# Kernel optimization log

Hardware: AMD Instinct MI355X
Metric: run time of the kernel (lower is better)

The kernel has to match this reference:

```python
import jax, jax.numpy as jnp
import numpy as np

B, S, V, E, H = 256, 512, 800, 128, 256

def setup_inputs() -> dict:
    key = jax.random.key(0)
    ks = jax.random.split(key, 16)
    def rn(k, shape, scale=0.05):
        return jax.random.normal(k, shape, dtype=jnp.float32) * scale
    return {
        "x": jax.random.randint(ks[0], (B, S), 0, V),
        "emb": rn(ks[1], (V, E), 1.0),
        "Wih0": rn(ks[2], (4 * H, E)),
        "Whh0": rn(ks[3], (4 * H, H)),
        "bih0": rn(ks[4], (4 * H,)),
        "bhh0": rn(ks[5], (4 * H,)),
        "Wih1": rn(ks[6], (4 * H, H)),
        "Whh1": rn(ks[7], (4 * H, H)),
        "bih1": rn(ks[8], (4 * H,)),
        "bhh1": rn(ks[9], (4 * H,)),
        "ln_g": jnp.ones((H,), jnp.float32),
        "ln_b": jnp.zeros((H,), jnp.float32),
        "proj_W": rn(ks[10], (E, H)),
        "proj_b": rn(ks[11], (E,)),
    }

def _lstm_layer(x, Wih, Whh, bih, bhh):
    # x: [B, S, D]; returns full hidden sequence [B, S, H]
    b, s, _ = x.shape
    h0 = jnp.zeros((b, H), x.dtype)
    c0 = jnp.zeros((b, H), x.dtype)
    # precompute input projections for all timesteps: [S, B, 4H]
    xp = jnp.einsum("bsd,gd->sbg", x, Wih) + bih + bhh

    def step(carry, xp_t):
        h, c = carry
        gates = xp_t + h @ Whh.T  # [B, 4H]
        i, f, g, o = jnp.split(gates, 4, axis=-1)  # torch gate order i,f,g,o
        i = jax.nn.sigmoid(i)
        f = jax.nn.sigmoid(f)
        g = jnp.tanh(g)
        o = jax.nn.sigmoid(o)
        c = f * c + i * g
        h = o * jnp.tanh(c)
        return (h, c), h

    (_, _), hs = jax.lax.scan(step, (h0, c0), xp)
    return hs.transpose(1, 0, 2)  # [B, S, H]

def reference(x, emb, Wih0, Whh0, bih0, bhh0, Wih1, Whh1, bih1, bhh1, ln_g, ln_b, proj_W, proj_b):
    table = emb.at[0].set(0.0)  # padding_idx=0
    e = table[x]  # [B, S, E]
    h1 = _lstm_layer(e, Wih0, Whh0, bih0, bhh0)
    h2 = _lstm_layer(h1, Wih1, Whh1, bih1, bhh1)
    hn = h2[:, -1, :]  # h_n[-1]: last layer, final timestep [B, H]
    mu = jnp.mean(hn, axis=-1, keepdims=True)
    var = jnp.mean(jnp.square(hn - mu), axis=-1, keepdims=True)
    y = (hn - mu) * jax.lax.rsqrt(var + 1e-5) * ln_g + ln_b
    return y @ proj_W.T + proj_b  # [B, 128]
```

## Files before the change

kernel.cpp:

```cpp
#include <hip/hip_runtime.h>
#include <hip/hip_bf16.h>


typedef unsigned short u16;
typedef unsigned int   u32;
using short8 = __attribute__((ext_vector_type(8))) short;
using f32x4  = __attribute__((ext_vector_type(4))) float;

#define NB 256
#define NS 512
#define NE 128
#define NH 256
#define NG 1024

#define WLDS_FRAGS 18
#define HOFF 147456
#define SCAN_LDS (HOFF + 2 * 16 * NH * 2)

#define L2E     1.4426950408889634f
#define TWO_L2E 2.8853900817779268f

__device__ __forceinline__ u16 f2b(float x) {
  __hip_bfloat16 h = __float2bfloat16(x);
  return __builtin_bit_cast(u16, h);
}
__device__ __forceinline__ float b2f(u16 u) {
  return __builtin_bit_cast(float, (u32)u << 16);
}
__device__ __forceinline__ float ex2(float x)  { return __builtin_amdgcn_exp2f(x); }
__device__ __forceinline__ float ex2n(float x) { return __builtin_amdgcn_exp2f(-x); }
__device__ __forceinline__ float rcpa(float x) { return __builtin_amdgcn_rcpf(x); }

__global__ __launch_bounds__(256) void prep_weights(
    const float* Wih0, const float* Whh0, const float* bih0, const float* bhh0,
    const float* Wih1, const float* Whh1, const float* bih1, const float* bhh1,
    u16* wih0b, u16* whh0b, u16* wih1b, u16* whh1b, float* bc0, float* bc1) {
  int stride = gridDim.x * blockDim.x;
  int tid = blockIdx.x * blockDim.x + threadIdx.x;
  for (int i = tid; i < NG * NE; i += stride) {
    float s = (((i >> 7) >> 8) == 2) ? TWO_L2E : L2E;
    wih0b[i] = f2b(Wih0[i] * s);
  }
  for (int i = tid; i < NG * NH; i += stride) {
    float s = (((i >> 8) >> 8) == 2) ? TWO_L2E : L2E;
    whh0b[i] = f2b(Whh0[i] * s);
    wih1b[i] = f2b(Wih1[i] * s);
    whh1b[i] = f2b(Whh1[i] * s);
  }
  for (int i = tid; i < NG; i += stride) {
    float s = ((i >> 8) == 2) ? TWO_L2E : L2E;
    bc0[i] = (bih0[i] + bhh0[i]) * s;
    bc1[i] = (bih1[i] + bhh1[i]) * s;
  }
}

__global__ __launch_bounds__(256) void embed_chunk(const int* __restrict__ x,
                                                   const float* __restrict__ emb,
                                                   u16* __restrict__ ebuf, int t0) {
  int gid = blockIdx.x * 256 + threadIdx.x;
  int d4 = gid & 31;
  int sb = gid >> 5;
  int b  = sb & (NB - 1);
  int sl = sb >> 8;
  int tok = x[b * NS + (t0 + sl)];
  float4 v = make_float4(0.f, 0.f, 0.f, 0.f);
  if (tok != 0) v = *(const float4*)(emb + (size_t)tok * NE + d4 * 4);
  ushort4 o;
  o.x = f2b(v.x); o.y = f2b(v.y); o.z = f2b(v.z); o.w = f2b(v.w);
  *(ushort4*)(ebuf + (size_t)sb * NE + d4 * 4) = o;
}

template <int K>
__global__ __launch_bounds__(256) void xp_gemm(const u16* __restrict__ A,
                                               const u16* __restrict__ W,
                                               const float* __restrict__ bias,
                                               u16* __restrict__ Cout) {
  __shared__ __align__(16) char lds[2 * 128 * 80];
  char* Asm = lds;
  char* Bsm = lds + 128 * 80;
  int tid = threadIdx.x;
  int w = tid >> 6, l = tid & 63;
  int hi = l >> 4, lo = l & 15;
  int mblk = blockIdx.x >> 3, nblk = blockIdx.x & 7;
  size_t arow0 = (size_t)mblk * 128;
  int g0 = nblk * 128;
  int wm = (w >> 1) * 64, wn = (w & 1) * 64;
  f32x4 acc[4][4] = {};
  int r = tid >> 1, cp = tid & 1;

  for (int k0 = 0; k0 < K; k0 += 32) {
    int4 a0 = *(const int4*)(A + (arow0 + r) * K + k0 + cp * 16);
    int4 a1 = *(const int4*)(A + (arow0 + r) * K + k0 + cp * 16 + 8);
    int4 b0 = *(const int4*)(W + (size_t)(g0 + r) * K + k0 + cp * 16);
    int4 b1 = *(const int4*)(W + (size_t)(g0 + r) * K + k0 + cp * 16 + 8);
    *(int4*)(Asm + r * 80 + cp * 32)      = a0;
    *(int4*)(Asm + r * 80 + cp * 32 + 16) = a1;
    *(int4*)(Bsm + r * 80 + cp * 32)      = b0;
    *(int4*)(Bsm + r * 80 + cp * 32 + 16) = b1;
    __syncthreads();
    short8 af[4], bfr[4];
#pragma unroll
    for (int mt = 0; mt < 4; ++mt)
      af[mt] = *(const short8*)(Asm + (wm + mt * 16 + lo) * 80 + hi * 16);
#pragma unroll
    for (int nt = 0; nt < 4; ++nt)
      bfr[nt] = *(const short8*)(Bsm + (wn + nt * 16 + lo) * 80 + hi * 16);
#pragma unroll
    for (int mt = 0; mt < 4; ++mt)
#pragma unroll
      for (int nt = 0; nt < 4; ++nt)
        acc[mt][nt] = __builtin_amdgcn_mfma_f32_16x16x32_bf16(af[mt], bfr[nt], acc[mt][nt], 0, 0, 0);
    __syncthreads();
  }
#pragma unroll
  for (int nt = 0; nt < 4; ++nt) {
    int gc = g0 + wn + nt * 16 + lo;
    float bv = bias[gc];
    int ws_ = (gc >> 4) & 7, mts = gc >> 7, his = (gc >> 2) & 3, rs = gc & 3;
    size_t gbase = ((size_t)(ws_ * 8 + mts) << 8) + (size_t)(his * 16) * 4 + rs;
#pragma unroll
    for (int mt = 0; mt < 4; ++mt) {
      size_t row = arow0 + wm + mt * 16 + hi * 4;
#pragma unroll
      for (int rr = 0; rr < 4; ++rr) {
        size_t rw = row + rr;
        int t = (int)(rw >> 8), ba = (int)(rw & 255);
        size_t e = ((size_t)(t * 16 + (ba >> 4)) << 14) + gbase + (size_t)(ba & 15) * 4;
        Cout[e] = f2b(acc[mt][nt][rr] + bv);
      }
    }
  }
}

__global__ __launch_bounds__(512, 2)
void scan_stage(const u16* __restrict__ xpA, const u16* __restrict__ whhA,
                u16* __restrict__ houtA, float* __restrict__ hsA,
                float* __restrict__ csA, int firstA, int activeA,
                const u16* __restrict__ xpB, const u16* __restrict__ whhB,
                float* __restrict__ hsB, float* __restrict__ csB,
                int firstB, int activeB, int T) {
  extern __shared__ __align__(16) char smem[];
  int bid = blockIdx.x;
  int roleB = bid >> 4;
  if (roleB ? !activeB : !activeA) return;
  const u16* xp      = roleB ? xpB  : xpA;
  const u16* whh     = roleB ? whhB : whhA;
  u16*       hout    = roleB ? (u16*)0 : houtA;
  float*     h_state = roleB ? hsB : hsA;
  float*     c_state = roleB ? csB : csA;
  int        first   = roleB ? firstB : firstA;
  int bgi = bid & 15;
  int bg = bgi * 16;

  int tid = threadIdx.x;
  int w = tid >> 6, l = tid & 63;
  int hi = l >> 4, lo = l & 15;

  int wbase = w * (WLDS_FRAGS * 1024) + l * 16;
  short8 wfv[8][5];
  short8 wfv2[6];
#pragma unroll
  for (int mt = 0; mt < 8; ++mt) {
#pragma unroll
    for (int p = 0; p < 8; ++p) {
      const u16* src = whh + (size_t)(16 * (w + 8 * mt) + lo) * NH + p * 32 + hi * 8;
      short8 v = *(const short8*)src;
      if (p < 2)                 *(short8*)(smem + wbase + (p * 8 + mt) * 1024) = v;
      else if (p == 2 && mt < 2) *(short8*)(smem + wbase + (16 + mt) * 1024) = v;
      else if (p == 2)           wfv2[mt - 2] = v;
      else                       wfv[mt][p - 3] = v;
    }
  }

  float c[2][4];
  if (first) {
    for (int i = tid; i < 16 * NH / 2; i += 512) ((u32*)(smem + HOFF))[i] = 0;
#pragma unroll
    for (int g = 0; g < 2; ++g)
#pragma unroll
      for (int r = 0; r < 4; ++r) c[g][r] = 0.0f;
  } else {
    for (int i = tid; i < 16 * NH; i += 512) {
      int b = i >> 8, k = i & 255;
      int p = k >> 5, hp = (k >> 3) & 3, kp = k & 7;
      int xx = hp * 16 + b;
      u16 hb = f2b(h_state[(size_t)(bg + b) * NH + k]);
      *(u16*)(smem + HOFF + p * 1024 + (xx ^ ((xx >> 3) & 7)) * 16 + kp * 2) = hb;
    }
#pragma unroll
    for (int g = 0; g < 2; ++g)
#pragma unroll
      for (int r = 0; r < 4; ++r) {
        int j = 16 * w + 128 * g + hi * 4 + r;
        c[g][r] = c_state[(size_t)(bg + lo) * NH + j];
      }
  }
  __syncthreads();

  int rdoff = (l ^ ((l >> 3) & 7)) * 16;
  int wroff[2];
#pragma unroll
  for (int g = 0; g < 2; ++g) {
    int xx = (2 * (w & 1) + (hi >> 1)) * 16 + lo;
    wroff[g] = (4 * g + (w >> 1)) * 1024 + (xx ^ ((xx >> 3) & 7)) * 16 + 8 * (hi & 1);
  }
  int bq = tid >> 5, kc = tid & 31;
  int xw = (kc & 3) * 16 + bq;
  int wboff = (kc >> 2) * 1024 + (xw ^ ((xw >> 3) & 7)) * 16;
  size_t wb_glob = (size_t)(bg + bq) * NH + kc * 8;

  const u16* xpp = xp + ((size_t)(bgi * 8 + w) * 2048) + (size_t)l * 4;

  ushort4 xq[8];
#pragma unroll
  for (int mt = 0; mt < 8; ++mt) xq[mt] = *(const ushort4*)(xpp + mt * 256);

  f32x4 acc[8];
  for (int t = 0; t < T; ++t) {
    int rbase = HOFF + ((t & 1) << 13);
    int wbbase = HOFF + ((~t & 1) << 13);
#pragma unroll
    for (int mt = 0; mt < 8; ++mt) {
      f32x4 a;
      a[0] = b2f(xq[mt].x); a[1] = b2f(xq[mt].y);
      a[2] = b2f(xq[mt].z); a[3] = b2f(xq[mt].w);
      acc[mt] = a;
    }
    xpp += 262144;
#pragma unroll
    for (int mt = 0; mt < 8; ++mt) xq[mt] = *(const ushort4*)(xpp + mt * 256);
#pragma unroll
    for (int p = 0; p < 8; ++p) {
      short8 bf = *(const short8*)(smem + rbase + rdoff + p * 1024);
#pragma unroll
      for (int mt = 0; mt < 8; ++mt) {
        short8 af;
        if (p < 2)                 af = *(const short8*)(smem + wbase + (p * 8 + mt) * 1024);
        else if (p == 2 && mt < 2) af = *(const short8*)(smem + wbase + (16 + mt) * 1024);
        else if (p == 2)           af = wfv2[mt - 2];
        else                       af = wfv[mt][p - 3];
        acc[mt] = __builtin_amdgcn_mfma_f32_16x16x32_bf16(af, bf, acc[mt], 0, 0, 0);
      }
    }
#pragma unroll
    for (int g = 0; g < 2; ++g) {
      float hv[4];
#pragma unroll
      for (int r = 0; r < 4; ++r) {
        float iv = rcpa(1.0f + ex2n(acc[g][r]));
        float fv = rcpa(1.0f + ex2n(acc[2 + g][r]));
        float gv = 1.0f - 2.0f * rcpa(ex2(acc[4 + g][r]) + 1.0f);
        float ov = rcpa(1.0f + ex2n(acc[6 + g][r]));
        float cc = fv * c[g][r] + iv * gv;
        c[g][r] = cc;
        float th = 1.0f - 2.0f * rcpa(ex2(cc * TWO_L2E) + 1.0f);
        hv[r] = ov * th;
      }
      u32 d0, d1;
      asm("v_cvt_pk_bf16_f32 %0, %1, %2" : "=v"(d0) : "v"(hv[0]), "v"(hv[1]));
      asm("v_cvt_pk_bf16_f32 %0, %1, %2" : "=v"(d1) : "v"(hv[2]), "v"(hv[3]));
      uint2 hw; hw.x = d0; hw.y = d1;
      *(uint2*)(smem + wbbase + wroff[g]) = hw;
    }
    __syncthreads();
    if (hout) {
      int4 hv4 = *(const int4*)(smem + wbbase + wboff);
      *(int4*)(hout + wb_glob + ((size_t)t << 16)) = hv4;
    }
  }

  int fbuf = HOFF + ((T & 1) << 13);
#pragma unroll
  for (int g = 0; g < 2; ++g) {
    ushort4 hv4 = *(const ushort4*)(smem + fbuf + wroff[g]);
    int j = 16 * w + 128 * g + 4 * hi;
    u16 hb[4] = {hv4.x, hv4.y, hv4.z, hv4.w};
#pragma unroll
    for (int r = 0; r < 4; ++r) {
      h_state[(size_t)(bg + lo) * NH + j + r] = b2f(hb[r]);
      c_state[(size_t)(bg + lo) * NH + j + r] = c[g][r];
    }
  }
}

__global__ __launch_bounds__(256) void ln_proj(const float* __restrict__ hn,
                                               const float* __restrict__ lng,
                                               const float* __restrict__ lnb,
                                               const float* __restrict__ pW,
                                               const float* __restrict__ pb,
                                               float* __restrict__ out) {
  __shared__ __align__(16) float nbuf[NH];
  __shared__ float red[8];
  int b = blockIdx.x, tid = threadIdx.x;
  float v = hn[(size_t)b * NH + tid];
  float s = v, s2 = v * v;
#pragma unroll
  for (int o = 32; o > 0; o >>= 1) {
    s  += __shfl_down(s, o);
    s2 += __shfl_down(s2, o);
  }
  if ((tid & 63) == 0) { red[tid >> 6] = s; red[4 + (tid >> 6)] = s2; }
  __syncthreads();
  if (tid == 0) {
    red[0] = red[0] + red[1] + red[2] + red[3];
    red[4] = red[4] + red[5] + red[6] + red[7];
  }
  __syncthreads();
  float mean = red[0] * (1.0f / NH);
  float var  = red[4] * (1.0f / NH) - mean * mean;
  float rs = rsqrtf(var + 1e-5f);
  nbuf[tid] = (v - mean) * rs * lng[tid] + lnb[tid];
  __syncthreads();
  if (tid < NE) {
    float a = pb[tid];
    const float* wr = pW + (size_t)tid * NH;
#pragma unroll 4
    for (int j = 0; j < NH; ++j) a = fmaf(nbuf[j], wr[j], a);
    out[(size_t)b * NE + tid] = a;
  }
}

extern "C" void kernel_launch(void* const* d_in, const int* in_sizes, int n_in,
                              void* d_out, int out_size, void* d_ws, size_t ws_size,
                              hipStream_t stream) {
  const int*   x     = (const int*)d_in[0];
  const float* emb   = (const float*)d_in[1];
  const float* Wih0  = (const float*)d_in[2];
  const float* Whh0  = (const float*)d_in[3];
  const float* bih0  = (const float*)d_in[4];
  const float* bhh0  = (const float*)d_in[5];
  const float* Wih1  = (const float*)d_in[6];
  const float* Whh1  = (const float*)d_in[7];
  const float* bih1  = (const float*)d_in[8];
  const float* bhh1  = (const float*)d_in[9];
  const float* ln_g  = (const float*)d_in[10];
  const float* ln_b  = (const float*)d_in[11];
  const float* projW = (const float*)d_in[12];
  const float* projb = (const float*)d_in[13];

  hipFuncSetAttribute((const void*)scan_stage,
                      hipFuncAttributeMaxDynamicSharedMemorySize, SCAN_LDS);

  const size_t FIXED = 2891776;
  int T = 128;
  while (T > 4 && FIXED + (size_t)T * 1179648 > ws_size) T >>= 1;
  int nch = NS / T;

  char* ws = (char*)d_ws;
  u16*   xpA   = (u16*)(ws);
  u16*   xpB   = (u16*)(ws + (size_t)T * 524288);
  u16*   iobuf = (u16*)(ws + (size_t)T * 1048576);
  char*  wbase = ws + (size_t)T * 1179648;
  u16*   wih0b = (u16*)(wbase);
  u16*   whh0b = (u16*)(wbase + 262144);
  u16*   wih1b = (u16*)(wbase + 786432);
  u16*   whh1b = (u16*)(wbase + 1310720);
  float* bc0   = (float*)(wbase + 1835008);
  float* bc1   = (float*)(wbase + 1839104);
  float* hs0   = (float*)(wbase + 1843200);
  float* cs0   = (float*)(wbase + 2105344);
  float* hs1   = (float*)(wbase + 2367488);
  float* cs1   = (float*)(wbase + 2629632);

  prep_weights<<<256, 256, 0, stream>>>(Wih0, Whh0, bih0, bhh0, Wih1, Whh1, bih1, bhh1,
                                        wih0b, whh0b, wih1b, whh1b, bc0, bc1);
  embed_chunk<<<T * 32, 256, 0, stream>>>(x, emb, iobuf, 0);
  xp_gemm<NE><<<T * 16, 256, 0, stream>>>(iobuf, wih0b, bc0, xpA);

  for (int s = 0; s <= nch; ++s) {
    int aA = (s < nch) ? 1 : 0;
    int aB = (s >= 1) ? 1 : 0;
    scan_stage<<<32, 512, SCAN_LDS, stream>>>(
        xpA, whh0b, iobuf, hs0, cs0, (s == 0) ? 1 : 0, aA,
        xpB, whh1b, hs1, cs1, (s == 1) ? 1 : 0, aB, T);
    if (s < nch) {
      xp_gemm<NH><<<T * 16, 256, 0, stream>>>(iobuf, wih1b, bc1, xpB);
      if (s + 1 < nch) {
        embed_chunk<<<T * 32, 256, 0, stream>>>(x, emb, iobuf, (s + 1) * T);
        xp_gemm<NE><<<T * 16, 256, 0, stream>>>(iobuf, wih0b, bc0, xpA);
      }
    }
  }
  ln_proj<<<NB, 256, 0, stream>>>(hs1, ln_g, ln_b, projW, projb, (float*)d_out);
}
```

Measured before the change: 1.678 ms.

## Overlap next-chunk layer-0 embedding+projection GEMM inside scan kernel blocks

Adds 32 extra blocks to the scan launch that compute the next chunk's layer-0 input projection, with the embedding gather fused into the GEMM's A-tile load. They write into a double-buffered xpA. This removes the separate embed_chunk and xp_gemm launches from the serial chain and runs that GEMM concurrently with the latency-bound recurrence on otherwise idle CUs. The chunk size drops from 128 to 64 to fit the extra buffer, which doubles the number of serial scan launches, and the GEMM blocks may contend with the scan blocks for bandwidth.

Result: no change. 1.653 ms (-1.5%).

```diff
diff --git a/kernel.cpp b/kernel.cpp
--- a/kernel.cpp
+++ b/kernel.cpp
@@ -138,9 +138,85 @@
                 float* __restrict__ csA, int firstA, int activeA,
                 const u16* __restrict__ xpB, const u16* __restrict__ whhB,
                 float* __restrict__ hsB, float* __restrict__ csB,
-                int firstB, int activeB, int T) {
+                int firstB, int activeB,
+                const int* __restrict__ x, const float* __restrict__ emb,
+                const u16* __restrict__ wih0b, const float* __restrict__ bc0,
+                u16* __restrict__ xpC, int t0c, int activeC, int T) {
   extern __shared__ __align__(16) char smem[];
   int bid = blockIdx.x;
+  int tid = threadIdx.x;
+
+  if (bid >= 32) {
+    if (!activeC) return;
+    int team = tid >> 8, tt = tid & 255;
+    char* Asm = smem + team * 40960;
+    char* Bsm = Asm + 20480;
+    int wq = tt >> 6, lq = tt & 63;
+    int hiq = lq >> 4, loq = lq & 15;
+    int wm = (wq >> 1) * 64, wn = (wq & 1) * 64;
+    int r = tt >> 1, cp = tt & 1;
+    int njobs = T * 16;
+    for (int j = (bid - 32) * 2 + team; j < njobs; j += 64) {
+      int mblk = j >> 3, nblk = j & 7;
+      size_t arow0 = (size_t)mblk * 128;
+      int g0 = nblk * 128;
+      f32x4 acc[4][4] = {};
+      int rw = (int)(arow0 + r);
+      int sl = rw >> 8, ba = rw & 255;
+      int tok = x[ba * NS + t0c + sl];
+      const float* erow = emb + (size_t)tok * NE;
+      for (int k0 = 0; k0 < NE; k0 += 32) {
+        const float* src = erow + k0 + cp * 16;
+        u32 pk[8];
+#pragma unroll
+        for (int q = 0; q < 8; ++q) {
+          float a = src[2 * q], b = src[2 * q + 1];
+          if (tok == 0) { a = 0.0f; b = 0.0f; }
+          pk[q] = (u32)f2b(a) | ((u32)f2b(b) << 16);
+        }
+        *(int4*)(Asm + r * 80 + cp * 32)      = *(int4*)&pk[0];
+        *(int4*)(Asm + r * 80 + cp * 32 + 16) = *(int4*)&pk[4];
+        int4 b0 = *(const int4*)(wih0b + (size_t)(g0 + r) * NE + k0 + cp * 16);
+        int4 b1 = *(const int4*)(wih0b + (size_t)(g0 + r) * NE + k0 + cp * 16 + 8);
+        *(int4*)(Bsm + r * 80 + cp * 32)      = b0;
+        *(int4*)(Bsm + r * 80 + cp * 32 + 16) = b1;
+        __syncthreads();
+        short8 af[4], bfr[4];
+#pragma unroll
+        for (int mt = 0; mt < 4; ++mt)
+          af[mt] = *(const short8*)(Asm + (wm + mt * 16 + loq) * 80 + hiq * 16);
+#pragma unroll
+        for (int nt = 0; nt < 4; ++nt)
+          bfr[nt] = *(const short8*)(Bsm + (wn + nt * 16 + loq) * 80 + hiq * 16);
+#pragma unroll
+        for (int mt = 0; mt < 4; ++mt)
+#pragma unroll
+          for (int nt = 0; nt < 4; ++nt)
+            acc[mt][nt] = __builtin_amdgcn_mfma_f32_16x16x32_bf16(af[mt], bfr[nt], acc[mt][nt], 0, 0, 0);
+        __syncthreads();
+      }
+#pragma unroll
+      for (int nt = 0; nt < 4; ++nt) {
+        int gc = g0 + wn + nt * 16 + loq;
+        float bv = bc0[gc];
+        int ws_ = (gc >> 4) & 7, mts = gc >> 7, his = (gc >> 2) & 3, rs = gc & 3;
+        size_t gbase = ((size_t)(ws_ * 8 + mts) << 8) + (size_t)(his * 16) * 4 + rs;
+#pragma unroll
+        for (int mt = 0; mt < 4; ++mt) {
+          size_t row = arow0 + wm + mt * 16 + hiq * 4;
+#pragma unroll
+          for (int rr = 0; rr < 4; ++rr) {
+            size_t rw2 = row + rr;
+            int t = (int)(rw2 >> 8), ba2 = (int)(rw2 & 255);
+            size_t e = ((size_t)(t * 16 + (ba2 >> 4)) << 14) + gbase + (size_t)(ba2 & 15) * 4;
+            xpC[e] = f2b(acc[mt][nt][rr] + bv);
+          }
+        }
+      }
+    }
+    return;
+  }
+
   int roleB = bid >> 4;
   if (roleB ? !activeB : !activeA) return;
   const u16* xp      = roleB ? xpB  : xpA;
@@ -152,7 +228,6 @@
   int bgi = bid & 15;
   int bg = bgi * 16;
 
-  int tid = threadIdx.x;
   int w = tid >> 6, l = tid & 63;
   int hi = l >> 4, lo = l & 15;
 
@@ -342,15 +417,16 @@
                       hipFuncAttributeMaxDynamicSharedMemorySize, SCAN_LDS);
 
   const size_t FIXED = 2891776;
-  int T = 128;
-  while (T > 4 && FIXED + (size_t)T * 1179648 > ws_size) T >>= 1;
+  int T = 64;
+  while (T > 4 && FIXED + (size_t)T * 1703936 > ws_size) T >>= 1;
   int nch = NS / T;
 
   char* ws = (char*)d_ws;
-  u16*   xpA   = (u16*)(ws);
-  u16*   xpB   = (u16*)(ws + (size_t)T * 524288);
-  u16*   iobuf = (u16*)(ws + (size_t)T * 1048576);
-  char*  wbase = ws + (size_t)T * 1179648;
+  u16*   xpA0  = (u16*)(ws);
+  u16*   xpA1  = (u16*)(ws + (size_t)T * 524288);
+  u16*   xpB   = (u16*)(ws + (size_t)T * 1048576);
+  u16*   iobuf = (u16*)(ws + (size_t)T * 1572864);
+  char*  wbase = ws + (size_t)T * 1703936;
   u16*   wih0b = (u16*)(wbase);
   u16*   whh0b = (u16*)(wbase + 262144);
   u16*   wih1b = (u16*)(wbase + 786432);
@@ -361,24 +437,23 @@
   float* cs0   = (float*)(wbase + 2105344);
   float* hs1   = (float*)(wbase + 2367488);
   float* cs1   = (float*)(wbase + 2629632);
+  u16*   xpA[2] = {xpA0, xpA1};
 
   prep_weights<<<256, 256, 0, stream>>>(Wih0, Whh0, bih0, bhh0, Wih1, Whh1, bih1, bhh1,
                                         wih0b, whh0b, wih1b, whh1b, bc0, bc1);
   embed_chunk<<<T * 32, 256, 0, stream>>>(x, emb, iobuf, 0);
-  xp_gemm<NE><<<T * 16, 256, 0, stream>>>(iobuf, wih0b, bc0, xpA);
+  xp_gemm<NE><<<T * 16, 256, 0, stream>>>(iobuf, wih0b, bc0, xpA0);
 
   for (int s = 0; s <= nch; ++s) {
     int aA = (s < nch) ? 1 : 0;
     int aB = (s >= 1) ? 1 : 0;
-    scan_stage<<<32, 512, SCAN_LDS, stream>>>(
-        xpA, whh0b, iobuf, hs0, cs0, (s == 0) ? 1 : 0, aA,
-        xpB, whh1b, hs1, cs1, (s == 1) ? 1 : 0, aB, T);
+    int aC = (s + 1 < nch) ? 1 : 0;
+    scan_stage<<<64, 512, SCAN_LDS, stream>>>(
+        xpA[s & 1], whh0b, iobuf, hs0, cs0, (s == 0) ? 1 : 0, aA,
+        xpB, whh1b, hs1, cs1, (s == 1) ? 1 : 0, aB,
+        x, emb, wih0b, bc0, xpA[(s + 1) & 1], (s + 1) * T, aC, T);
     if (s < nch) {
       xp_gemm<NH><<<T * 16, 256, 0, stream>>>(iobuf, wih1b, bc1, xpB);
-      if (s + 1 < nch) {
-        embed_chunk<<<T * 32, 256, 0, stream>>>(x, emb, iobuf, (s + 1) * T);
-        xp_gemm<NE><<<T * 16, 256, 0, stream>>>(iobuf, wih0b, bc0, xpA);
-      }
     }
   }
   ln_proj<<<NB, 256, 0, stream>>>(hs1, ln_g, ln_b, projW, projb, (float*)d_out);
```
